# Kernel optimization log

Measured on AMD Instinct MI355X. Metric: run time of the kernel, lower is better.

Reference implementation:

```python
import jax, jax.numpy as jnp
import numpy as np

N_NODES = 100000
N_EDGES = 1600000
DIM = 64
N_LAYERS = 6


def setup_inputs() -> dict:
    key = jax.random.key(0)
    ks = jax.random.split(key, 4)
    x = jax.random.normal(ks[0], (N_NODES, DIM), dtype=jnp.float32)
    edge_index = jax.random.randint(ks[1], (2, N_EDGES), 0, N_NODES, dtype=jnp.int64)
    # SAGEConv params per layer: lin_l (neighbor, with bias), lin_r (root, no bias)
    Wl = jax.random.normal(ks[2], (N_LAYERS, DIM, DIM), dtype=jnp.float32) * 0.05
    bl = jnp.zeros((N_LAYERS, DIM), dtype=jnp.float32)
    Wr = jax.random.normal(ks[3], (N_LAYERS, DIM, DIM), dtype=jnp.float32) * 0.05
    return {"x": x, "edge_index": edge_index, "Wl": Wl, "bl": bl, "Wr": Wr}


def reference(x, edge_index, Wl, bl, Wr):
    src, dst = edge_index[0], edge_index[1]
    n = x.shape[0]

    def sage(h, W_l, b_l, W_r):
        # gather neighbor features [E, D], scatter-max into dst nodes [N, D]
        agg = jax.ops.segment_max(h[src], dst, num_segments=n)
        # nodes with no in-edges get -inf from segment_max -> 0 (PyG convention)
        agg = jnp.where(jnp.isneginf(agg), jnp.zeros((), h.dtype), agg)
        return agg @ W_l.T + b_l + h @ W_r.T

    h = x
    for i in range(N_LAYERS):
        h = sage(h, Wl[i], bl[i], Wr[i])
        if i < N_LAYERS - 1:
            h = jax.nn.relu(h)
        # dropout (p=0.1) is identity in eval mode
    return h
```

## Files before the change

kernel.cpp:

```cpp
#include <hip/hip_runtime.h>
#include <hip/hip_bf16.h>
#include <math.h>

#define DIM 64

typedef _Float16 half_t;
typedef __attribute__((ext_vector_type(8))) _Float16 half8;
typedef __attribute__((ext_vector_type(4))) _Float16 h16x4;
typedef __attribute__((ext_vector_type(4))) float f32x4;

__device__ __forceinline__ half8 hmax8(half8 a, half8 b) {
    return __builtin_elementwise_max(a, b);
}
__device__ __forceinline__ half8 shfl_xor_h8(half8 v, int mask) {
    union { half8 h; int i[4]; } u;
    u.h = v;
#pragma unroll
    for (int k = 0; k < 4; ++k) u.i[k] = __shfl_xor(u.i[k], mask);
    return u.h;
}


__global__ void kbcnt(const int* __restrict__ ei, int E, int* __restrict__ gcnt) {
    __shared__ int h[256];
    int t = threadIdx.x;
    h[t] = 0;
    __syncthreads();
    for (int e = blockIdx.x * 256 + t; e < E; e += gridDim.x * 256)
        atomicAdd(&h[ei[E + e] >> 9], 1);
    __syncthreads();
    if (h[t]) atomicAdd(&gcnt[t], h[t]);
}

__global__ void kbscan(const int* __restrict__ gcnt, int* __restrict__ gbs,
                       int* __restrict__ gbc, int NB, int E,
                       int* __restrict__ rs, int N) {
    __shared__ int sm[256];
    int t = threadIdx.x;
    int v = (t < NB) ? gcnt[t] : 0;
    sm[t] = v;
    __syncthreads();
    for (int off = 1; off < 256; off <<= 1) {
        int add = (t >= off) ? sm[t - off] : 0;
        __syncthreads();
        sm[t] += add;
        __syncthreads();
    }
    int excl = sm[t] - v;
    if (t < NB) { gbs[t] = excl; gbc[t] = excl; }
    if (t == NB - 1) gbs[NB] = excl + v;
    if (t == 0) rs[N] = E;
}

__global__ void kbin(const int* __restrict__ ei, int E,
                     int* __restrict__ gbc, int* __restrict__ pairs, int NB) {
    __shared__ int hist[256];
    __shared__ int basep[256];
    const int t = threadIdx.x;
    const int c0 = blockIdx.x * 4096;
    hist[t] = 0;
    __syncthreads();
    int s[16], d[16];
#pragma unroll
    for (int i = 0; i < 16; ++i) {
        int e = c0 + i * 256 + t;
        if (e < E) {
            s[i] = ei[e];
            d[i] = ei[E + e];
            atomicAdd(&hist[d[i] >> 9], 1);
        } else d[i] = -1;
    }
    __syncthreads();
    if (t < NB) {
        basep[t] = atomicAdd(&gbc[t], hist[t]);
        hist[t] = 0;
    }
    __syncthreads();
#pragma unroll
    for (int i = 0; i < 16; ++i) {
        if (d[i] >= 0) {
            int b = d[i] >> 9;
            int off = atomicAdd(&hist[b], 1);
            pairs[basep[b] + off] = (s[i] << 9) | (d[i] & 511);
        }
    }
}

__global__ void __launch_bounds__(256) kfinal(
        const int* __restrict__ pairs, const int* __restrict__ gbs,
        int* __restrict__ rs, int* __restrict__ ssrc, int N) {
    __shared__ int lcnt[512];
    __shared__ int lcur[512];
    __shared__ int ps[256];
    const int b = blockIdx.x;
    const int t = threadIdx.x;
    const int n0 = b << 9;
    const int e0 = gbs[b], e1 = gbs[b + 1];
    lcnt[t] = 0;
    lcnt[t + 256] = 0;
    __syncthreads();
    for (int e = e0 + t; e < e1; e += 256)
        atomicAdd(&lcnt[pairs[e] & 511], 1);
    __syncthreads();
    int c0 = lcnt[2 * t], c1 = lcnt[2 * t + 1];
    int sum = c0 + c1;
    ps[t] = sum;
    __syncthreads();
    for (int off = 1; off < 256; off <<= 1) {
        int add = (t >= off) ? ps[t - off] : 0;
        __syncthreads();
        ps[t] += add;
        __syncthreads();
    }
    int excl = ps[t] - sum;
    lcur[2 * t] = excl;
    lcur[2 * t + 1] = excl + c0;
    int n = n0 + 2 * t;
    if (n < N) rs[n] = e0 + excl;
    if (n + 1 < N) rs[n + 1] = e0 + excl + c0;
    __syncthreads();
    for (int e = e0 + t; e < e1; e += 256) {
        int p = pairs[e];
        int pos = atomicAdd(&lcur[p & 511], 1);
        ssrc[e0 + pos] = (int)((unsigned)p >> 9) << 7;
    }
}


__global__ void kcvt(const float* __restrict__ x, half_t* __restrict__ phi,
                     half_t* __restrict__ plo, int n4) {
    int i = blockIdx.x * blockDim.x + threadIdx.x;
    if (i < n4) {
        f32x4 v = ((const f32x4*)x)[i];
        h16x4 hi, lo;
#pragma unroll
        for (int c = 0; c < 4; ++c) {
            hi[c] = (half_t)v[c];
            lo[c] = (half_t)(v[c] - (float)hi[c]);
        }
        ((h16x4*)phi)[i] = hi;
        ((h16x4*)plo)[i] = lo;
    }
}


__global__ void kprepw(const float* __restrict__ Wl, const float* __restrict__ Wr,
                       half_t* __restrict__ Bf) {
    int id = blockIdx.x * blockDim.x + threadIdx.x;
    if (id >= 6 * 4 * 4 * 64 * 8) return;
    int i = id & 7;
    int lane = (id >> 3) & 63;
    int t = (id >> 9) & 3;
    int s = (id >> 11) & 3;
    int layer = id >> 13;
    int k = s * 32 + (lane >> 4) * 8 + i;
    int j = t * 16 + (lane & 15);
    float v = (k < 64) ? Wl[(layer * 64 + j) * 64 + k]
                       : Wr[(layer * 64 + j) * 64 + (k - 64)];
    half_t hi = (half_t)v;
    half_t lo = (half_t)(v - (float)hi);
    int f = (s * 4 + t) * 2;
    int base = layer * 16384 + f * 512 + lane * 8 + i;
    Bf[base] = hi;
    Bf[base + 512] = lo;
}


__global__ void kagg(const half_t* __restrict__ h16, const int* __restrict__ rs,
                     const int* __restrict__ soff, half_t* __restrict__ agg16, int N) {
    int w = (blockIdx.x * blockDim.x + threadIdx.x) >> 6;
    int lane = threadIdx.x & 63;
    if (w >= N) return;
    int g = lane >> 3, sub = lane & 7;
    const char* hb = (const char*)h16 + sub * 16;
    int beg = rs[w], end = rs[w + 1];
    const half_t NEG = (half_t)(-65504.0f);
    half8 m0 = {NEG, NEG, NEG, NEG, NEG, NEG, NEG, NEG}, m1 = m0;
    for (int base = beg; base < end; base += 64) {
        int cnt = end - base;
        if (cnt > 64) cnt = 64;
        int sv = (lane < cnt) ? soff[base + lane] : 0;
        int j = 0;
        for (; j + 15 < cnt; j += 16) {
            int o0 = __shfl(sv, j + g);
            int o1 = __shfl(sv, j + 8 + g);
            half8 v0 = *(const half8*)(hb + o0);
            half8 v1 = *(const half8*)(hb + o1);
            m0 = hmax8(m0, v0);
            m1 = hmax8(m1, v1);
        }
        for (; j + 7 < cnt; j += 8) {
            int o0 = __shfl(sv, j + g);
            m0 = hmax8(m0, *(const half8*)(hb + o0));
        }
        if (j < cnt) {
            int jg = j + g;
            if (jg >= cnt) jg = cnt - 1;
            int o0 = __shfl(sv, jg);
            m0 = hmax8(m0, *(const half8*)(hb + o0));
        }
    }
    half8 m = hmax8(m0, m1);
    m = hmax8(m, shfl_xor_h8(m, 8));
    m = hmax8(m, shfl_xor_h8(m, 16));
    m = hmax8(m, shfl_xor_h8(m, 32));
    if (g == 0) {
        if (end <= beg) {
            half8 z = {(half_t)0.f, (half_t)0.f, (half_t)0.f, (half_t)0.f,
                       (half_t)0.f, (half_t)0.f, (half_t)0.f, (half_t)0.f};
            m = z;
        }
        *(half8*)((char*)agg16 + (size_t)w * 128 + sub * 16) = m;
    }
}


__global__ void __launch_bounds__(256, 2) kgemm(
        const half_t* __restrict__ agg16, const half_t* __restrict__ hhi,
        const half_t* __restrict__ hlo, const half_t* __restrict__ Bf,
        const float* __restrict__ bias, float* __restrict__ out32,
        half_t* __restrict__ ohi, half_t* __restrict__ olo, int N, int last) {
    const int lane = threadIdx.x & 63;
    const int quad = lane >> 4;
    const int lrow = lane & 15;
    const int wv = (blockIdx.x * blockDim.x + threadIdx.x) >> 6;
    const int nwv = (gridDim.x * blockDim.x) >> 6;
    const int ntiles = (N + 15) >> 4;

    const half8* __restrict__ Bp = (const half8*)Bf;
    half8 bh[4][4], bl[4][4];
#pragma unroll
    for (int s = 0; s < 4; ++s)
#pragma unroll
        for (int t = 0; t < 4; ++t) {
            int f = (s * 4 + t) * 2;
            bh[s][t] = Bp[f * 64 + lane];
            bl[s][t] = Bp[f * 64 + 64 + lane];
        }

    float bs[4];
#pragma unroll
    for (int t = 0; t < 4; ++t) bs[t] = bias[t * 16 + lrow];

    for (int tile = wv; tile < ntiles; tile += nwv) {
        const int m0 = tile << 4;
        int row = m0 + lrow;
        if (row >= N) row = N - 1;
        const char* pa = (const char*)agg16 + (size_t)row * 128 + quad * 16;
        const char* ph = (const char*)hhi   + (size_t)row * 128 + quad * 16;
        const char* pl = (const char*)hlo   + (size_t)row * 128 + quad * 16;
        half8 Aa0 = *(const half8*)(pa);
        half8 Aa1 = *(const half8*)(pa + 64);
        half8 Hh0 = *(const half8*)(ph);
        half8 Hh1 = *(const half8*)(ph + 64);
        half8 Hl0 = *(const half8*)(pl);
        half8 Hl1 = *(const half8*)(pl + 64);

        f32x4 acc[4] = {{0.f, 0.f, 0.f, 0.f}, {0.f, 0.f, 0.f, 0.f},
                        {0.f, 0.f, 0.f, 0.f}, {0.f, 0.f, 0.f, 0.f}};
#pragma unroll
        for (int t = 0; t < 4; ++t) {
            acc[t] = __builtin_amdgcn_mfma_f32_16x16x32_f16(Aa0, bh[0][t], acc[t], 0, 0, 0);
            acc[t] = __builtin_amdgcn_mfma_f32_16x16x32_f16(Aa0, bl[0][t], acc[t], 0, 0, 0);
            acc[t] = __builtin_amdgcn_mfma_f32_16x16x32_f16(Aa1, bh[1][t], acc[t], 0, 0, 0);
            acc[t] = __builtin_amdgcn_mfma_f32_16x16x32_f16(Aa1, bl[1][t], acc[t], 0, 0, 0);
            acc[t] = __builtin_amdgcn_mfma_f32_16x16x32_f16(Hh0, bh[2][t], acc[t], 0, 0, 0);
            acc[t] = __builtin_amdgcn_mfma_f32_16x16x32_f16(Hl0, bh[2][t], acc[t], 0, 0, 0);
            acc[t] = __builtin_amdgcn_mfma_f32_16x16x32_f16(Hh0, bl[2][t], acc[t], 0, 0, 0);
            acc[t] = __builtin_amdgcn_mfma_f32_16x16x32_f16(Hh1, bh[3][t], acc[t], 0, 0, 0);
            acc[t] = __builtin_amdgcn_mfma_f32_16x16x32_f16(Hl1, bh[3][t], acc[t], 0, 0, 0);
            acc[t] = __builtin_amdgcn_mfma_f32_16x16x32_f16(Hh1, bl[3][t], acc[t], 0, 0, 0);
        }

#pragma unroll
        for (int t = 0; t < 4; ++t) {
            int col = t * 16 + lrow;
#pragma unroll
            for (int r = 0; r < 4; ++r) {
                int orow = m0 + quad * 4 + r;
                if (orow < N) {
                    float v = acc[t][r] + bs[t];
                    if (!last) {
                        v = fmaxf(v, 0.0f);
                        half_t hi = (half_t)v;
                        half_t lo = (half_t)(v - (float)hi);
                        ohi[(size_t)orow * DIM + col] = hi;
                        olo[(size_t)orow * DIM + col] = lo;
                    } else {
                        out32[(size_t)orow * DIM + col] = v;
                    }
                }
            }
        }
    }
}


extern "C" void kernel_launch(void* const* d_in, const int* in_sizes, int n_in,
                              void* d_out, int out_size, void* d_ws, size_t ws_size,
                              hipStream_t stream) {
    const float* x  = (const float*)d_in[0];
    const int*   ei = (const int*)d_in[1];
    const float* Wl = (const float*)d_in[2];
    const float* bl = (const float*)d_in[3];
    const float* Wr = (const float*)d_in[4];
    int N = in_sizes[0] / DIM;
    int E = in_sizes[1] / 2;

    size_t nd = (size_t)N * DIM;
    half_t* p0hi  = (half_t*)d_ws;
    half_t* p0lo  = p0hi + nd;
    half_t* p1hi  = p0lo + nd;
    half_t* p1lo  = p1hi + nd;
    half_t* agg16 = p1lo + nd;
    int*    rs    = (int*)(agg16 + nd);
    int*    ssrc  = rs + (N + 4);
    int*    gcnt  = ssrc + E;
    int*    gbs   = gcnt + 256;
    int*    gbc   = gbs + 260;
    half_t* Bf    = (half_t*)(gbc + 256);

    int NB = (N + 511) >> 9;
    int* pairs = (int*)agg16;

    hipMemsetAsync(gcnt, 0, 256 * sizeof(int), stream);
    kbcnt<<<640, 256, 0, stream>>>(ei, E, gcnt);
    kbscan<<<1, 256, 0, stream>>>(gcnt, gbs, gbc, NB, E, rs, N);
    kbin<<<(E + 4095) / 4096, 256, 0, stream>>>(ei, E, gbc, pairs, NB);
    kfinal<<<NB, 256, 0, stream>>>(pairs, gbs, rs, ssrc, N);
    kprepw<<<(6 * 4 * 4 * 64 * 8 + 255) / 256, 256, 0, stream>>>(Wl, Wr, Bf);
    kcvt<<<((int)(nd / 4) + 255) / 256, 256, 0, stream>>>(x, p0hi, p0lo, (int)(nd / 4));

    for (int l = 0; l < 6; ++l) {
        half_t* ihi = (l & 1) ? p1hi : p0hi;
        half_t* ilo = (l & 1) ? p1lo : p0lo;
        half_t* xhi = (l & 1) ? p0hi : p1hi;
        half_t* xlo = (l & 1) ? p0lo : p1lo;
        int last = (l == 5);
        kagg<<<(N + 3) / 4, 256, 0, stream>>>(ihi, rs, ssrc, agg16, N);
        kgemm<<<512, 256, 0, stream>>>(agg16, ihi, ilo, Bf + l * 16384, bl + l * 64,
                                       (float*)d_out, xhi, xlo, N, last);
    }
}
```

Measured before the change: 461.9 us.

## Fuse neighbor max-aggregation into GEMM kernel and drop low-half activation split

Merges the separate aggregation and GEMM kernels into one per-layer kernel. Each lane gathers neighbor rows for its own tile row and max-reduces them in registers, then feeds the result straight into MFMA with weights staged in shared memory. It also drops the hi/lo fp16 split of the activations, so they are stored as plain fp16, which halves activation traffic but loses precision. The fused gather reads each row's edges serially per lane instead of cooperatively across a wavefront, which may lower memory parallelism and cause load imbalance.

New measurement: 617.7 us. 33.7% more time.

```diff
diff --git a/kernel.cpp b/kernel.cpp
--- a/kernel.cpp
+++ b/kernel.cpp
@@ -11,13 +11,6 @@
 
 __device__ __forceinline__ half8 hmax8(half8 a, half8 b) {
     return __builtin_elementwise_max(a, b);
-}
-__device__ __forceinline__ half8 shfl_xor_h8(half8 v, int mask) {
-    union { half8 h; int i[4]; } u;
-    u.h = v;
-#pragma unroll
-    for (int k = 0; k < 4; ++k) u.i[k] = __shfl_xor(u.i[k], mask);
-    return u.h;
 }
 
 
@@ -127,19 +120,14 @@
 }
 
 
-__global__ void kcvt(const float* __restrict__ x, half_t* __restrict__ phi,
-                     half_t* __restrict__ plo, int n4) {
+__global__ void kcvt(const float* __restrict__ x, half_t* __restrict__ phi, int n4) {
     int i = blockIdx.x * blockDim.x + threadIdx.x;
     if (i < n4) {
         f32x4 v = ((const f32x4*)x)[i];
-        h16x4 hi, lo;
-#pragma unroll
-        for (int c = 0; c < 4; ++c) {
-            hi[c] = (half_t)v[c];
-            lo[c] = (half_t)(v[c] - (float)hi[c]);
-        }
+        h16x4 hi;
+#pragma unroll
+        for (int c = 0; c < 4; ++c) hi[c] = (half_t)v[c];
         ((h16x4*)phi)[i] = hi;
-        ((h16x4*)plo)[i] = lo;
     }
 }
 
@@ -166,110 +154,78 @@
 }
 
 
-__global__ void kagg(const half_t* __restrict__ h16, const int* __restrict__ rs,
-                     const int* __restrict__ soff, half_t* __restrict__ agg16, int N) {
-    int w = (blockIdx.x * blockDim.x + threadIdx.x) >> 6;
-    int lane = threadIdx.x & 63;
-    if (w >= N) return;
-    int g = lane >> 3, sub = lane & 7;
-    const char* hb = (const char*)h16 + sub * 16;
-    int beg = rs[w], end = rs[w + 1];
-    const half_t NEG = (half_t)(-65504.0f);
-    half8 m0 = {NEG, NEG, NEG, NEG, NEG, NEG, NEG, NEG}, m1 = m0;
-    for (int base = beg; base < end; base += 64) {
-        int cnt = end - base;
-        if (cnt > 64) cnt = 64;
-        int sv = (lane < cnt) ? soff[base + lane] : 0;
-        int j = 0;
-        for (; j + 15 < cnt; j += 16) {
-            int o0 = __shfl(sv, j + g);
-            int o1 = __shfl(sv, j + 8 + g);
-            half8 v0 = *(const half8*)(hb + o0);
-            half8 v1 = *(const half8*)(hb + o1);
-            m0 = hmax8(m0, v0);
-            m1 = hmax8(m1, v1);
-        }
-        for (; j + 7 < cnt; j += 8) {
-            int o0 = __shfl(sv, j + g);
-            m0 = hmax8(m0, *(const half8*)(hb + o0));
-        }
-        if (j < cnt) {
-            int jg = j + g;
-            if (jg >= cnt) jg = cnt - 1;
-            int o0 = __shfl(sv, jg);
-            m0 = hmax8(m0, *(const half8*)(hb + o0));
-        }
-    }
-    half8 m = hmax8(m0, m1);
-    m = hmax8(m, shfl_xor_h8(m, 8));
-    m = hmax8(m, shfl_xor_h8(m, 16));
-    m = hmax8(m, shfl_xor_h8(m, 32));
-    if (g == 0) {
-        if (end <= beg) {
-            half8 z = {(half_t)0.f, (half_t)0.f, (half_t)0.f, (half_t)0.f,
-                       (half_t)0.f, (half_t)0.f, (half_t)0.f, (half_t)0.f};
-            m = z;
-        }
-        *(half8*)((char*)agg16 + (size_t)w * 128 + sub * 16) = m;
-    }
-}
-
-
-__global__ void __launch_bounds__(256, 2) kgemm(
-        const half_t* __restrict__ agg16, const half_t* __restrict__ hhi,
-        const half_t* __restrict__ hlo, const half_t* __restrict__ Bf,
-        const float* __restrict__ bias, float* __restrict__ out32,
-        half_t* __restrict__ ohi, half_t* __restrict__ olo, int N, int last) {
-    const int lane = threadIdx.x & 63;
+__global__ void __launch_bounds__(256, 4) klayer(
+        const half_t* __restrict__ hin, const int* __restrict__ rs,
+        const int* __restrict__ soff, const half_t* __restrict__ Bf,
+        const float* __restrict__ bias, half_t* __restrict__ hout,
+        float* __restrict__ out32, int N, int last) {
+    __shared__ half8 Bs[2048];
+    const int tid = threadIdx.x;
+    const half8* __restrict__ Bg = (const half8*)Bf;
+#pragma unroll
+    for (int i = 0; i < 8; ++i) Bs[i * 256 + tid] = Bg[i * 256 + tid];
+    __syncthreads();
+
+    const int lane = tid & 63;
     const int quad = lane >> 4;
     const int lrow = lane & 15;
-    const int wv = (blockIdx.x * blockDim.x + threadIdx.x) >> 6;
+    const int wv = (blockIdx.x * blockDim.x + tid) >> 6;
     const int nwv = (gridDim.x * blockDim.x) >> 6;
     const int ntiles = (N + 15) >> 4;
-
-    const half8* __restrict__ Bp = (const half8*)Bf;
-    half8 bh[4][4], bl[4][4];
-#pragma unroll
-    for (int s = 0; s < 4; ++s)
-#pragma unroll
-        for (int t = 0; t < 4; ++t) {
-            int f = (s * 4 + t) * 2;
-            bh[s][t] = Bp[f * 64 + lane];
-            bl[s][t] = Bp[f * 64 + 64 + lane];
-        }
-
-    float bs[4];
-#pragma unroll
-    for (int t = 0; t < 4; ++t) bs[t] = bias[t * 16 + lrow];
+    const char* hb = (const char*)hin + quad * 16;
+
+    float bs_[4];
+#pragma unroll
+    for (int t = 0; t < 4; ++t) bs_[t] = bias[t * 16 + lrow];
+
+    const half_t NEG = (half_t)(-65504.0f);
+    const half8 NEG8 = {NEG, NEG, NEG, NEG, NEG, NEG, NEG, NEG};
+    const half8 Z8 = {(half_t)0.f, (half_t)0.f, (half_t)0.f, (half_t)0.f,
+                      (half_t)0.f, (half_t)0.f, (half_t)0.f, (half_t)0.f};
 
     for (int tile = wv; tile < ntiles; tile += nwv) {
         const int m0 = tile << 4;
         int row = m0 + lrow;
         if (row >= N) row = N - 1;
-        const char* pa = (const char*)agg16 + (size_t)row * 128 + quad * 16;
-        const char* ph = (const char*)hhi   + (size_t)row * 128 + quad * 16;
-        const char* pl = (const char*)hlo   + (size_t)row * 128 + quad * 16;
-        half8 Aa0 = *(const half8*)(pa);
-        half8 Aa1 = *(const half8*)(pa + 64);
-        half8 Hh0 = *(const half8*)(ph);
-        half8 Hh1 = *(const half8*)(ph + 64);
-        half8 Hl0 = *(const half8*)(pl);
-        half8 Hl1 = *(const half8*)(pl + 64);
+        int beg = rs[row], end = rs[row + 1];
+        int lastE = end - 1;
+
+        half8 a0 = NEG8, a1 = NEG8, b0 = NEG8, b1 = NEG8;
+        half8 c0 = NEG8, c1 = NEG8, d0 = NEG8, d1 = NEG8;
+        for (int e = beg; e < end; e += 4) {
+            int e1 = (e + 1 <= lastE) ? e + 1 : lastE;
+            int e2 = (e + 2 <= lastE) ? e + 2 : lastE;
+            int e3 = (e + 3 <= lastE) ? e + 3 : lastE;
+            int o0 = soff[e], o1 = soff[e1], o2 = soff[e2], o3 = soff[e3];
+            a0 = hmax8(a0, *(const half8*)(hb + o0));
+            a1 = hmax8(a1, *(const half8*)(hb + o0 + 64));
+            b0 = hmax8(b0, *(const half8*)(hb + o1));
+            b1 = hmax8(b1, *(const half8*)(hb + o1 + 64));
+            c0 = hmax8(c0, *(const half8*)(hb + o2));
+            c1 = hmax8(c1, *(const half8*)(hb + o2 + 64));
+            d0 = hmax8(d0, *(const half8*)(hb + o3));
+            d1 = hmax8(d1, *(const half8*)(hb + o3 + 64));
+        }
+        half8 A0 = hmax8(hmax8(a0, b0), hmax8(c0, d0));
+        half8 A1 = hmax8(hmax8(a1, b1), hmax8(c1, d1));
+        if (end <= beg) { A0 = Z8; A1 = Z8; }
+
+        const char* ph = (const char*)hin + (size_t)row * 128 + quad * 16;
+        half8 H0 = *(const half8*)(ph);
+        half8 H1 = *(const half8*)(ph + 64);
 
         f32x4 acc[4] = {{0.f, 0.f, 0.f, 0.f}, {0.f, 0.f, 0.f, 0.f},
                         {0.f, 0.f, 0.f, 0.f}, {0.f, 0.f, 0.f, 0.f}};
 #pragma unroll
         for (int t = 0; t < 4; ++t) {
-            acc[t] = __builtin_amdgcn_mfma_f32_16x16x32_f16(Aa0, bh[0][t], acc[t], 0, 0, 0);
-            acc[t] = __builtin_amdgcn_mfma_f32_16x16x32_f16(Aa0, bl[0][t], acc[t], 0, 0, 0);
-            acc[t] = __builtin_amdgcn_mfma_f32_16x16x32_f16(Aa1, bh[1][t], acc[t], 0, 0, 0);
-            acc[t] = __builtin_amdgcn_mfma_f32_16x16x32_f16(Aa1, bl[1][t], acc[t], 0, 0, 0);
-            acc[t] = __builtin_amdgcn_mfma_f32_16x16x32_f16(Hh0, bh[2][t], acc[t], 0, 0, 0);
-            acc[t] = __builtin_amdgcn_mfma_f32_16x16x32_f16(Hl0, bh[2][t], acc[t], 0, 0, 0);
-            acc[t] = __builtin_amdgcn_mfma_f32_16x16x32_f16(Hh0, bl[2][t], acc[t], 0, 0, 0);
-            acc[t] = __builtin_amdgcn_mfma_f32_16x16x32_f16(Hh1, bh[3][t], acc[t], 0, 0, 0);
-            acc[t] = __builtin_amdgcn_mfma_f32_16x16x32_f16(Hl1, bh[3][t], acc[t], 0, 0, 0);
-            acc[t] = __builtin_amdgcn_mfma_f32_16x16x32_f16(Hh1, bl[3][t], acc[t], 0, 0, 0);
+            acc[t] = __builtin_amdgcn_mfma_f32_16x16x32_f16(A0, Bs[((0 * 4 + t) * 2 + 0) * 64 + lane], acc[t], 0, 0, 0);
+            acc[t] = __builtin_amdgcn_mfma_f32_16x16x32_f16(A0, Bs[((0 * 4 + t) * 2 + 1) * 64 + lane], acc[t], 0, 0, 0);
+            acc[t] = __builtin_amdgcn_mfma_f32_16x16x32_f16(A1, Bs[((1 * 4 + t) * 2 + 0) * 64 + lane], acc[t], 0, 0, 0);
+            acc[t] = __builtin_amdgcn_mfma_f32_16x16x32_f16(A1, Bs[((1 * 4 + t) * 2 + 1) * 64 + lane], acc[t], 0, 0, 0);
+            acc[t] = __builtin_amdgcn_mfma_f32_16x16x32_f16(H0, Bs[((2 * 4 + t) * 2 + 0) * 64 + lane], acc[t], 0, 0, 0);
+            acc[t] = __builtin_amdgcn_mfma_f32_16x16x32_f16(H0, Bs[((2 * 4 + t) * 2 + 1) * 64 + lane], acc[t], 0, 0, 0);
+            acc[t] = __builtin_amdgcn_mfma_f32_16x16x32_f16(H1, Bs[((3 * 4 + t) * 2 + 0) * 64 + lane], acc[t], 0, 0, 0);
+            acc[t] = __builtin_amdgcn_mfma_f32_16x16x32_f16(H1, Bs[((3 * 4 + t) * 2 + 1) * 64 + lane], acc[t], 0, 0, 0);
         }
 
 #pragma unroll
@@ -279,13 +235,10 @@
             for (int r = 0; r < 4; ++r) {
                 int orow = m0 + quad * 4 + r;
                 if (orow < N) {
-                    float v = acc[t][r] + bs[t];
+                    float v = acc[t][r] + bs_[t];
                     if (!last) {
                         v = fmaxf(v, 0.0f);
-                        half_t hi = (half_t)v;
-                        half_t lo = (half_t)(v - (float)hi);
-                        ohi[(size_t)orow * DIM + col] = hi;
-                        olo[(size_t)orow * DIM + col] = lo;
+                        hout[(size_t)orow * DIM + col] = (half_t)v;
                     } else {
                         out32[(size_t)orow * DIM + col] = v;
                     }
@@ -308,12 +261,9 @@
     int E = in_sizes[1] / 2;
 
     size_t nd = (size_t)N * DIM;
-    half_t* p0hi  = (half_t*)d_ws;
-    half_t* p0lo  = p0hi + nd;
-    half_t* p1hi  = p0lo + nd;
-    half_t* p1lo  = p1hi + nd;
-    half_t* agg16 = p1lo + nd;
-    int*    rs    = (int*)(agg16 + nd);
+    half_t* p0    = (half_t*)d_ws;
+    half_t* p1    = p0 + nd;
+    int*    rs    = (int*)(p1 + nd);
     int*    ssrc  = rs + (N + 4);
     int*    gcnt  = ssrc + E;
     int*    gbs   = gcnt + 256;
@@ -321,7 +271,7 @@
     half_t* Bf    = (half_t*)(gbc + 256);
 
     int NB = (N + 511) >> 9;
-    int* pairs = (int*)agg16;
+    int* pairs = (int*)p1;
 
     hipMemsetAsync(gcnt, 0, 256 * sizeof(int), stream);
     kbcnt<<<640, 256, 0, stream>>>(ei, E, gcnt);
@@ -329,16 +279,13 @@
     kbin<<<(E + 4095) / 4096, 256, 0, stream>>>(ei, E, gbc, pairs, NB);
     kfinal<<<NB, 256, 0, stream>>>(pairs, gbs, rs, ssrc, N);
     kprepw<<<(6 * 4 * 4 * 64 * 8 + 255) / 256, 256, 0, stream>>>(Wl, Wr, Bf);
-    kcvt<<<((int)(nd / 4) + 255) / 256, 256, 0, stream>>>(x, p0hi, p0lo, (int)(nd / 4));
+    kcvt<<<((int)(nd / 4) + 255) / 256, 256, 0, stream>>>(x, p0, (int)(nd / 4));
 
     for (int l = 0; l < 6; ++l) {
-        half_t* ihi = (l & 1) ? p1hi : p0hi;
-        half_t* ilo = (l & 1) ? p1lo : p0lo;
-        half_t* xhi = (l & 1) ? p0hi : p1hi;
-        half_t* xlo = (l & 1) ? p0lo : p1lo;
+        half_t* ih = (l & 1) ? p1 : p0;
+        half_t* oh = (l & 1) ? p0 : p1;
         int last = (l == 5);
-        kagg<<<(N + 3) / 4, 256, 0, stream>>>(ihi, rs, ssrc, agg16, N);
-        kgemm<<<512, 256, 0, stream>>>(agg16, ihi, ilo, Bf + l * 16384, bl + l * 64,
-                                       (float*)d_out, xhi, xlo, N, last);
-    }
-}
+        klayer<<<1024, 256, 0, stream>>>(ih, rs, ssrc, Bf + l * 16384, bl + l * 64,
+                                         oh, (float*)d_out, N, last);
+    }
+}
```
